# Performance work log

Hardware: AMD Instinct MI355X
Metric: run time of the kernel (lower is better)

Reference implementation:

```python
import jax, jax.numpy as jnp
import numpy as np

B, C, H, W = 16, 64, 128, 128
C8 = C // 8


def setup_inputs() -> dict:
    key = jax.random.key(0)
    ks = jax.random.split(key, 8)
    s = 0.05
    return {
        "x": jax.random.normal(ks[0], (B, C, H, W), dtype=jnp.float32),
        "Wq": jax.random.normal(ks[1], (C8, C), dtype=jnp.float32) * s,
        "bq": jax.random.normal(ks[2], (C8,), dtype=jnp.float32) * s,
        "Wk": jax.random.normal(ks[3], (C8, C), dtype=jnp.float32) * s,
        "bk": jax.random.normal(ks[4], (C8,), dtype=jnp.float32) * s,
        "Wv": jax.random.normal(ks[5], (C, C), dtype=jnp.float32) * s,
        "bv": jax.random.normal(ks[6], (C,), dtype=jnp.float32) * s,
        "gamma": jnp.zeros((1,), dtype=jnp.float32),
    }


def _criss_cross(x, Wq, bq, Wk, bk, Wv, bv, gamma):
    # 1x1 convs == channel-mixing matmuls
    q = jnp.einsum("bchw,oc->bohw", x, Wq) + bq[None, :, None, None]  # [B,C8,H,W]
    k = jnp.einsum("bchw,oc->bohw", x, Wk) + bk[None, :, None, None]  # [B,C8,H,W]
    v = jnp.einsum("bchw,oc->bohw", x, Wv) + bv[None, :, None, None]  # [B,C,H,W]

    h = x.shape[2]
    # column (H-axis) attention scores; diagonal masked to -inf
    energy_H = jnp.einsum("bchw,bciw->bhwi", q, k)  # [B,H,W,H]
    diag = jnp.eye(h, dtype=bool)[None, :, None, :]  # mask where query row == key row
    energy_H = jnp.where(diag, -jnp.inf, energy_H)
    # row (W-axis) attention scores
    energy_W = jnp.einsum("bchw,bchj->bhwj", q, k)  # [B,H,W,W]

    # joint softmax over concatenated H+W axis
    att = jax.nn.softmax(jnp.concatenate([energy_H, energy_W], axis=3), axis=3)
    att_H = att[:, :, :, :h]    # [B,H,W,H]
    att_W = att[:, :, :, h:]    # [B,H,W,W]

    out_H = jnp.einsum("bhwi,bciw->bchw", att_H, v)
    out_W = jnp.einsum("bhwj,bchj->bchw", att_W, v)
    return gamma[0] * (out_H + out_W) + x


def reference(x, Wq, bq, Wk, bk, Wv, bv, gamma):
    return _criss_cross(x, Wq, bq, Wk, bk, Wv, bv, gamma)
```

## Files before the change

kernel.cpp:

```cpp
#include <hip/hip_runtime.h>

#define HW 128
#define CC 64
#define C8V 8
#define NB 16

typedef _Float16 h1;
typedef _Float16 h2 __attribute__((ext_vector_type(2)));
typedef _Float16 half8 __attribute__((ext_vector_type(8)));
typedef float float16v __attribute__((ext_vector_type(16)));
typedef uint uv4 __attribute__((ext_vector_type(4)));

__device__ __forceinline__ uint packh2(float a, float b) {
#if __has_builtin(__builtin_amdgcn_cvt_pkrtz)
  return __builtin_bit_cast(uint, __builtin_amdgcn_cvt_pkrtz(a, b));
#else
  h2 v; v[0] = (h1)a; v[1] = (h1)b; return __builtin_bit_cast(uint, v);
#endif
}
__device__ __forceinline__ ushort f2h(float a) { h1 v = (h1)a; return __builtin_bit_cast(ushort, v); }
__device__ __forceinline__ float  h2f(ushort a) { return (float)__builtin_bit_cast(h1, a); }

__device__ __forceinline__ float16v mfma16(uv4 a, uv4 b, float16v c) {
  return __builtin_amdgcn_mfma_f32_32x32x16_f16(
      __builtin_bit_cast(half8, a), __builtin_bit_cast(half8, b), c, 0, 0, 0);
}

__global__ __launch_bounds__(256) void k_proj(
    const float* __restrict__ x,
    const float* __restrict__ Wq, const float* __restrict__ bq,
    const float* __restrict__ Wk, const float* __restrict__ bk,
    const float* __restrict__ Wv, const float* __restrict__ bv,
    ushort* __restrict__ q, ushort* __restrict__ k, ushort* __restrict__ v)
{
  alignas(16) __shared__ ushort smem[16128];
  __shared__ float bias_l[96];
  ushort* x_l = smem;
  ushort* W_l = smem + 128 * 72;

  int t = threadIdx.x;
  int lane = t & 63, wv = t >> 6;
  int b = blockIdx.x >> 7, r = blockIdx.x & 127;

  #pragma unroll
  for (int i = 0; i < 20; ++i) {
    int idx = t + 256 * i; int o_ = idx >> 6, c = idx & 63;
    float wval = (o_ < 8) ? Wq[o_ * 64 + c] : (o_ < 16) ? Wk[(o_ - 8) * 64 + c] : Wv[(o_ - 16) * 64 + c];
    W_l[o_ * 72 + c] = f2h(wval);
  }
  if (t < 96) bias_l[t] = (t < 8) ? bq[t] : (t < 16) ? bk[t - 8] : (t < 80) ? bv[t - 16] : 0.f;

  const float* xrow = x + (size_t)(b * CC) * (HW * HW) + (size_t)r * HW;
  #pragma unroll
  for (int i = 0; i < 8; ++i) {
    int idx = t + 256 * i; int c = idx >> 5, w4 = idx & 31;
    float4 xv = *(const float4*)(xrow + (size_t)c * (HW * HW) + w4 * 4);
    x_l[(w4 * 4 + 0) * 72 + c] = f2h(xv.x);
    x_l[(w4 * 4 + 1) * 72 + c] = f2h(xv.y);
    x_l[(w4 * 4 + 2) * 72 + c] = f2h(xv.z);
    x_l[(w4 * 4 + 3) * 72 + c] = f2h(xv.w);
  }
  __syncthreads();

  int w = 32 * wv + (lane & 31);
  float16v acc0 = {}, acc1 = {}, acc2 = {};
  #pragma unroll
  for (int ks = 0; ks < 4; ++ks) {
    int c0 = 8 * (lane >> 5) + 16 * ks;
    uv4 Bx = *(const uv4*)&x_l[w * 72 + c0];
    uv4 a0 = *(const uv4*)&W_l[((lane & 31) + 0) * 72 + c0];
    uv4 a1 = *(const uv4*)&W_l[((lane & 31) + 32) * 72 + c0];
    uv4 a2 = *(const uv4*)&W_l[((lane & 31) + 64) * 72 + c0];
    acc0 = mfma16(a0, Bx, acc0);
    acc1 = mfma16(a1, Bx, acc1);
    acc2 = mfma16(a2, Bx, acc2);
  }
  __syncthreads();

  ushort* o_l = smem;
  int hi = lane >> 5;
  #pragma unroll
  for (int reg = 0; reg < 16; ++reg) {
    int orow = (reg & 3) + 8 * (reg >> 2) + 4 * hi;
    o_l[(orow +  0) * 128 + w] = f2h(acc0[reg] + bias_l[orow]);
    o_l[(orow + 32) * 128 + w] = f2h(acc1[reg] + bias_l[orow + 32]);
    if (orow + 64 < 80)
      o_l[(orow + 64) * 128 + w] = f2h(acc2[reg] + bias_l[orow + 64]);
  }
  __syncthreads();

  ushort* qb = q + (size_t)(b * C8V) * (HW * HW) + (size_t)r * HW;
  ushort* kb = k + (size_t)(b * C8V) * (HW * HW) + (size_t)r * HW;
  ushort* vb = v + (size_t)(b * CC)  * (HW * HW) + (size_t)r * HW;
  #pragma unroll
  for (int i = 0; i < 5; ++i) {
    int idx = t + 256 * i; int o_ = idx >> 4, w8 = idx & 15;
    uv4 val = *(const uv4*)&o_l[o_ * 128 + w8 * 8];
    ushort* dst = (o_ < 8) ? qb + (size_t)o_ * (HW * HW)
                : (o_ < 16) ? kb + (size_t)(o_ - 8) * (HW * HW)
                            : vb + (size_t)(o_ - 16) * (HW * HW);
    *(uv4*)(dst + w8 * 8) = val;
  }
}

__global__ __launch_bounds__(256) void k_transpose_all(
    const ushort* __restrict__ q, ushort* __restrict__ qT,
    const ushort* __restrict__ k, ushort* __restrict__ kT,
    const ushort* __restrict__ v, ushort* __restrict__ vT)
{
  __shared__ ushort tl[128 * 130];
  int t = threadIdx.x;
  int p = blockIdx.x;
  const ushort* in; ushort* out;
  if (p < 128)      { size_t base = (size_t)p * (HW * HW);         in = q + base; out = qT + base; }
  else if (p < 256) { size_t base = (size_t)(p - 128) * (HW * HW); in = k + base; out = kT + base; }
  else              { size_t base = (size_t)(p - 256) * (HW * HW); in = v + base; out = vT + base; }
  const uint* ip = (const uint*)in;
  uint* op = (uint*)out;
  int c2 = t & 63;
  int r0 = t >> 6;
  for (int it = 0; it < 32; ++it) {
    int r = it * 4 + r0;
    uint val = ip[r * 64 + c2];
    *(uint*)&tl[r * 130 + c2 * 2] = val;
  }
  __syncthreads();
  for (int it = 0; it < 32; ++it) {
    int wcol = it * 4 + r0;
    int hh = c2 * 2;
    uint lo = tl[hh * 130 + wcol];
    uint hi = tl[(hh + 1) * 130 + wcol];
    op[wcol * 64 + c2] = lo | (hi << 16);
  }
}

__global__ __launch_bounds__(256) void k_attn_both(
    const ushort* __restrict__ q,  const ushort* __restrict__ kkn, const ushort* __restrict__ vn,
    const ushort* __restrict__ qT, const ushort* __restrict__ kkT, const ushort* __restrict__ vT,
    ushort* __restrict__ oW_, float* __restrict__ mW_, float* __restrict__ sW_,
    ushort* __restrict__ oH_, float* __restrict__ mH_, float* __restrict__ sH_)
{
  alignas(16) __shared__ ushort Q_l[128][16];
  alignas(16) __shared__ ushort K_l[128][16];
  alignas(16) __shared__ uint   V_l[64 * 64];

  int t = threadIdx.x;
  int lane = t & 63, wv = t >> 6;
  int hi = lane >> 5;
  int bid = blockIdx.x & 2047;
  bool maskf = blockIdx.x >= 2048;
  const ushort* qp = maskf ? qT : q;
  const ushort* kp = maskf ? kkT : kkn;
  const ushort* vp = maskf ? vT : vn;
  ushort* op = maskf ? oH_ : oW_;
  float* mo = maskf ? mH_ : mW_;
  float* so = maskf ? sH_ : sW_;

  int b = bid >> 7, r = bid & 127;
  size_t plane32 = (size_t)(HW * HW) / 2;

  if (t < 128) {
    *(uv4*)&Q_l[t][8] = (uv4){0, 0, 0, 0};
    *(uv4*)&K_l[t][8] = (uv4){0, 0, 0, 0};
  }
  const uint* qrow = (const uint*)qp + (size_t)(b * C8V) * plane32 + (size_t)r * 64;
  const uint* krow = (const uint*)kp + (size_t)(b * C8V) * plane32 + (size_t)r * 64;
  #pragma unroll
  for (int i = 0; i < 2; ++i) {
    int idx = t + 256 * i; int c = idx >> 6, w2 = idx & 63;
    uint qv = qrow[(size_t)c * plane32 + w2];
    Q_l[2 * w2][c] = (ushort)(qv & 0xffff); Q_l[2 * w2 + 1][c] = (ushort)(qv >> 16);
    uint kv = krow[(size_t)c * plane32 + w2];
    K_l[2 * w2][c] = (ushort)(kv & 0xffff); K_l[2 * w2 + 1][c] = (ushort)(kv >> 16);
  }
  const uint* vrow = (const uint*)vp + (size_t)(b * CC) * plane32 + (size_t)r * 64;
  #pragma unroll
  for (int i = 0; i < 16; ++i) {
    int idx = t + 256 * i; int c = idx >> 6, j2 = idx & 63;
    uint val = vrow[(size_t)c * plane32 + j2];
    uint byteoff = c * 256 + ((4 * j2) ^ ((c & 15) << 4));
    V_l[byteoff >> 2] = val;
  }
  __syncthreads();

  uv4 Bq = *(const uv4*)&Q_l[(lane & 31) + 32 * wv][hi * 8];
  float16v e[4];
  #pragma unroll
  for (int mt = 0; mt < 4; ++mt) {
    uv4 ka = *(const uv4*)&K_l[(lane & 31) + 32 * mt][hi * 8];
    float16v z = {};
    e[mt] = mfma16(ka, Bq, z);
  }

  int qg = 32 * wv + (lane & 31);
  float m = -INFINITY;
  #pragma unroll
  for (int mt = 0; mt < 4; ++mt) {
    #pragma unroll
    for (int reg = 0; reg < 16; ++reg) {
      float ev = e[mt][reg];
      if (maskf) {
        int key = 32 * mt + ((reg & 3) + 8 * (reg >> 2) + 4 * hi);
        ev = (key == qg) ? -INFINITY : ev;
        e[mt][reg] = ev;
      }
      m = fmaxf(m, ev);
    }
  }
  m = fmaxf(m, __shfl_xor(m, 32));
  float s = 0.f;
  #pragma unroll
  for (int mt = 0; mt < 4; ++mt) {
    #pragma unroll
    for (int reg = 0; reg < 16; ++reg) {
      float p = __expf(e[mt][reg] - m);
      e[mt][reg] = p;
      s += p;
    }
  }
  s += __shfl_xor(s, 32);
  if (lane < 32) {
    mo[(size_t)bid * HW + qg] = m;
    so[(size_t)bid * HW + qg] = s;
  }

  float16v acc0 = {}, acc1 = {};
  #pragma unroll
  for (int s8 = 0; s8 < 8; ++s8) {
    int mt = s8 >> 1, hf = s8 & 1;
    float p0 = e[mt][8 * hf + 0], p1 = e[mt][8 * hf + 1];
    float p2 = e[mt][8 * hf + 2], p3 = e[mt][8 * hf + 3];
    float p4 = e[mt][8 * hf + 4], p5 = e[mt][8 * hf + 5];
    float p6 = e[mt][8 * hf + 6], p7 = e[mt][8 * hf + 7];
    uint X = packh2(p0, p1), Y = packh2(p2, p3), Z = packh2(p4, p5), Wp = packh2(p6, p7);
    uint Xs = __shfl_xor(X, 32), Ys = __shfl_xor(Y, 32);
    uint Zs = __shfl_xor(Z, 32), Ws = __shfl_xor(Wp, 32);
    uv4 Bp;
    Bp[0] = (hi == 0) ? X  : Zs;
    Bp[1] = (hi == 0) ? Y  : Ws;
    Bp[2] = (hi == 0) ? Xs : Z;
    Bp[3] = (hi == 0) ? Ys : Wp;
    #pragma unroll
    for (int ct = 0; ct < 2; ++ct) {
      int c = (lane & 31) + 32 * ct;
      uint byteoff = c * 256 + ((16 * (hi + 2 * s8)) ^ ((c & 15) << 4));
      uv4 va = *(const uv4*)((const char*)V_l + byteoff);
      if (ct == 0) acc0 = mfma16(va, Bp, acc0);
      else         acc1 = mfma16(va, Bp, acc1);
    }
  }

  __syncthreads();
  ushort* o_l = (ushort*)V_l;
  int w = 32 * wv + (lane & 31);
  #pragma unroll
  for (int reg = 0; reg < 16; ++reg) {
    int c = (reg & 3) + 8 * (reg >> 2) + 4 * hi;
    o_l[(c +  0) * 128 + w] = f2h(acc0[reg]);
    o_l[(c + 32) * 128 + w] = f2h(acc1[reg]);
  }
  __syncthreads();
  ushort* ob = op + (size_t)(b * CC) * (HW * HW) + (size_t)r * HW;
  #pragma unroll
  for (int i = 0; i < 4; ++i) {
    int idx = t + 256 * i; int c = idx >> 4, w8 = idx & 15;
    *(uv4*)(ob + (size_t)c * (HW * HW) + w8 * 8) = *(const uv4*)&o_l[c * 128 + w8 * 8];
  }
}

__global__ __launch_bounds__(256) void k_alpha(
    const float* __restrict__ mH, const float* __restrict__ sH,
    const float* __restrict__ mW, const float* __restrict__ sW,
    ushort* __restrict__ aHT, ushort* __restrict__ aWn)
{
  __shared__ float mw_l[128 * 17], sw_l[128 * 17];
  __shared__ ushort aw_l[128 * 18];
  int t = threadIdx.x;
  int b = blockIdx.x >> 3, ws = blockIdx.x & 7;
  int w0 = ws * 16;
  const int PL = HW * HW;

  #pragma unroll
  for (int i = 0; i < 8; ++i) {
    int p = t + 256 * i;
    int w = p & 15, h = p >> 4;
    mw_l[h * 17 + w] = mW[(size_t)b * PL + h * HW + w0 + w];
    sw_l[h * 17 + w] = sW[(size_t)b * PL + h * HW + w0 + w];
  }
  __syncthreads();
  #pragma unroll
  for (int i = 0; i < 8; ++i) {
    int p = t + 256 * i;
    int h = p & 127, w = p >> 7;
    size_t tidx = (size_t)b * PL + (size_t)(w0 + w) * HW + h;
    float mh = mH[tidx], sh = sH[tidx];
    float mw = mw_l[h * 17 + w], sw = sw_l[h * 17 + w];
    float mm = fmaxf(mh, mw);
    float eh = __expf(mh - mm), ew = __expf(mw - mm);
    float inv = 1.f / (sh * eh + sw * ew);
    aHT[tidx] = f2h(eh * inv);
    aw_l[h * 18 + w] = f2h(ew * inv);
  }
  __syncthreads();
  #pragma unroll
  for (int i = 0; i < 8; ++i) {
    int p = t + 256 * i;
    int w = p & 15, h = p >> 4;
    aWn[(size_t)b * PL + (size_t)h * HW + w0 + w] = aw_l[h * 18 + w];
  }
}

__global__ __launch_bounds__(256) void k_merge(
    const ushort* __restrict__ oHT, const ushort* __restrict__ oW,
    const ushort* __restrict__ aHT, const ushort* __restrict__ aWn,
    const float* __restrict__ x, const float* __restrict__ gamma,
    float* __restrict__ out)
{
  alignas(16) __shared__ ushort otile[4 * 32 * 132];
  int t = threadIdx.x;
  int bid = blockIdx.x;
  int wsel = bid & 3, cg = (bid >> 2) & 15, b = bid >> 6;
  int w0 = wsel * 32;
  float g = gamma[0];
  const int PL = HW * HW;

  #pragma unroll
  for (int i = 0; i < 8; ++i) {
    int p = t + 256 * i;
    int ch = p >> 9, rest = p & 511;
    int w = rest >> 4, hg = rest & 15;
    size_t cbase = (size_t)(b * CC + cg * 4 + ch) * PL;
    uv4 ov = *(const uv4*)(oHT + cbase + (size_t)(w0 + w) * HW + hg * 8);
    uv4 av = *(const uv4*)(aHT + (size_t)b * PL + (size_t)(w0 + w) * HW + hg * 8);
    uv4 res;
    #pragma unroll
    for (int jj = 0; jj < 4; ++jj) {
      h2 o2 = __builtin_bit_cast(h2, ov[jj]);
      h2 a2 = __builtin_bit_cast(h2, av[jj]);
      res[jj] = __builtin_bit_cast(uint, o2 * a2);
    }
    *(uv4*)&otile[(ch * 32 + w) * 132 + hg * 8] = res;
  }
  __syncthreads();

  #pragma unroll
  for (int ch = 0; ch < 4; ++ch) {
    size_t cbase = (size_t)(b * CC + cg * 4 + ch) * PL;
    const ushort* otc = &otile[ch * 32 * 132];
    #pragma unroll
    for (int i = 0; i < 2; ++i) {
      int p = t + 256 * i;
      int w4 = p & 7, hh2 = p >> 3;
      float th0[4], th1[4];
      #pragma unroll
      for (int j = 0; j < 4; ++j) {
        uint pk = *(const uint*)&otc[(4 * w4 + j) * 132 + 2 * hh2];
        th0[j] = h2f((ushort)(pk & 0xffff));
        th1[j] = h2f((ushort)(pk >> 16));
      }
      #pragma unroll
      for (int rr = 0; rr < 2; ++rr) {
        int hh = 2 * hh2 + rr;
        const float* th = rr ? th1 : th0;
        size_t base = cbase + (size_t)hh * HW + w0 + 4 * w4;
        size_t abase = (size_t)b * PL + (size_t)hh * HW + w0 + 4 * w4;
        uint2 aw2 = *(const uint2*)(aWn + abase);
        uint2 ow2 = *(const uint2*)(oW + base);
        float4 xv = *(const float4*)(x + base);
        float4 res;
        res.x = g * (th[0] + h2f((ushort)(ow2.x & 0xffff)) * h2f((ushort)(aw2.x & 0xffff))) + xv.x;
        res.y = g * (th[1] + h2f((ushort)(ow2.x >> 16))    * h2f((ushort)(aw2.x >> 16)))    + xv.y;
        res.z = g * (th[2] + h2f((ushort)(ow2.y & 0xffff)) * h2f((ushort)(aw2.y & 0xffff))) + xv.z;
        res.w = g * (th[3] + h2f((ushort)(ow2.y >> 16))    * h2f((ushort)(aw2.y >> 16)))    + xv.w;
        *(float4*)(out + base) = res;
      }
    }
  }
}

extern "C" void kernel_launch(void* const* d_in, const int* in_sizes, int n_in,
                              void* d_out, int out_size, void* d_ws, size_t ws_size,
                              hipStream_t stream)
{
  const float* x     = (const float*)d_in[0];
  const float* Wq    = (const float*)d_in[1];
  const float* bq    = (const float*)d_in[2];
  const float* Wk    = (const float*)d_in[3];
  const float* bk    = (const float*)d_in[4];
  const float* Wv    = (const float*)d_in[5];
  const float* bv    = (const float*)d_in[6];
  const float* gamma = (const float*)d_in[7];
  float* out = (float*)d_out;

  char* w = (char*)d_ws;
  size_t np = (size_t)NB * HW * HW;
  ushort* q   = (ushort*)w;  w += np * C8V * 2;
  ushort* k   = (ushort*)w;  w += np * C8V * 2;
  ushort* qT  = (ushort*)w;  w += np * C8V * 2;
  ushort* kT  = (ushort*)w;  w += np * C8V * 2;
  ushort* v   = (ushort*)w;  w += np * CC * 2;
  ushort* vT  = (ushort*)w;  w += np * CC * 2;
  ushort* oW  = (ushort*)w;  w += np * CC * 2;
  ushort* oHT = (ushort*)w;  w += np * CC * 2;
  float* mW = (float*)w;  w += np * 4;
  float* sW = (float*)w;  w += np * 4;
  float* mH = (float*)w;  w += np * 4;
  float* sH = (float*)w;  w += np * 4;
  ushort* aHT = (ushort*)w; w += np * 2;
  ushort* aWn = (ushort*)w; w += np * 2;
  if ((size_t)(w - (char*)d_ws) > ws_size) return;

  k_proj<<<NB * HW, 256, 0, stream>>>(x, Wq, bq, Wk, bk, Wv, bv, q, k, v);
  k_transpose_all<<<256 + NB * CC, 256, 0, stream>>>(q, qT, k, kT, v, vT);
  k_attn_both<<<2 * NB * HW, 256, 0, stream>>>(q, k, v, qT, kT, vT,
                                               oW, mW, sW, oHT, mH, sH);
  k_alpha<<<NB * 8, 256, 0, stream>>>(mH, sH, mW, sW, aHT, aWn);
  k_merge<<<NB * 16 * 4, 256, 0, stream>>>(oHT, oW, aHT, aWn, x, gamma, out);
}
```

Measured before the change: 123.9 us.

## Store q/k pixel-major with zero padding to drop their transposes

The projection kernel now writes q and k in a per-pixel layout of 16 halfs (8 channels plus 8 zeros), so the attention kernel can load MFMA operands straight from global memory for both row and column passes. This removes the q/k transpose blocks and the q/k shared-memory staging in the attention kernel. The column pass now reads with a strided, less coalesced pattern, and q/k storage doubles in size because of the zero padding.

```diff
diff --git a/kernel.cpp b/kernel.cpp
--- a/kernel.cpp
+++ b/kernel.cpp
@@ -77,46 +77,50 @@
   }
   __syncthreads();
 
-  ushort* o_l = smem;
+  ushort* o_l  = smem;
+  ushort* qk_l = smem + 8192;
   int hi = lane >> 5;
+
+  {
+    int zw = t >> 1, sel = t & 1;
+    *(uv4*)&qk_l[zw * 40 + 8 + 16 * sel] = (uv4){0, 0, 0, 0};
+  }
+
   #pragma unroll
   for (int reg = 0; reg < 16; ++reg) {
     int orow = (reg & 3) + 8 * (reg >> 2) + 4 * hi;
-    o_l[(orow +  0) * 128 + w] = f2h(acc0[reg] + bias_l[orow]);
-    o_l[(orow + 32) * 128 + w] = f2h(acc1[reg] + bias_l[orow + 32]);
-    if (orow + 64 < 80)
-      o_l[(orow + 64) * 128 + w] = f2h(acc2[reg] + bias_l[orow + 64]);
-  }
-  __syncthreads();
-
-  ushort* qb = q + (size_t)(b * C8V) * (HW * HW) + (size_t)r * HW;
-  ushort* kb = k + (size_t)(b * C8V) * (HW * HW) + (size_t)r * HW;
-  ushort* vb = v + (size_t)(b * CC)  * (HW * HW) + (size_t)r * HW;
-  #pragma unroll
-  for (int i = 0; i < 5; ++i) {
+    float v0 = acc0[reg] + bias_l[orow];
+    if (orow < 8)       qk_l[w * 40 + orow] = f2h(v0);
+    else if (orow < 16) qk_l[w * 40 + 8 + orow] = f2h(v0);
+    else                o_l[(orow - 16) * 128 + w] = f2h(v0);
+    o_l[(orow + 16) * 128 + w] = f2h(acc1[reg] + bias_l[orow + 32]);
+    if (orow < 16)
+      o_l[(orow + 48) * 128 + w] = f2h(acc2[reg] + bias_l[orow + 64]);
+  }
+  __syncthreads();
+
+  size_t pixbase = (size_t)(b * HW + r) * HW * 16;
+  {
+    int pw = t >> 1, part = t & 1;
+    *(uv4*)(q + pixbase + t * 8) = *(const uv4*)&qk_l[pw * 40 + part * 8];
+    *(uv4*)(k + pixbase + t * 8) = *(const uv4*)&qk_l[pw * 40 + 16 + part * 8];
+  }
+  ushort* vb = v + (size_t)(b * CC) * (HW * HW) + (size_t)r * HW;
+  #pragma unroll
+  for (int i = 0; i < 4; ++i) {
     int idx = t + 256 * i; int o_ = idx >> 4, w8 = idx & 15;
-    uv4 val = *(const uv4*)&o_l[o_ * 128 + w8 * 8];
-    ushort* dst = (o_ < 8) ? qb + (size_t)o_ * (HW * HW)
-                : (o_ < 16) ? kb + (size_t)(o_ - 8) * (HW * HW)
-                            : vb + (size_t)(o_ - 16) * (HW * HW);
-    *(uv4*)(dst + w8 * 8) = val;
-  }
-}
-
-__global__ __launch_bounds__(256) void k_transpose_all(
-    const ushort* __restrict__ q, ushort* __restrict__ qT,
-    const ushort* __restrict__ k, ushort* __restrict__ kT,
-    const ushort* __restrict__ v, ushort* __restrict__ vT)
+    *(uv4*)(vb + (size_t)o_ * (HW * HW) + w8 * 8) = *(const uv4*)&o_l[o_ * 128 + w8 * 8];
+  }
+}
+
+__global__ __launch_bounds__(256) void k_transpose_v(const ushort* __restrict__ v,
+                                                     ushort* __restrict__ vT)
 {
   __shared__ ushort tl[128 * 130];
   int t = threadIdx.x;
-  int p = blockIdx.x;
-  const ushort* in; ushort* out;
-  if (p < 128)      { size_t base = (size_t)p * (HW * HW);         in = q + base; out = qT + base; }
-  else if (p < 256) { size_t base = (size_t)(p - 128) * (HW * HW); in = k + base; out = kT + base; }
-  else              { size_t base = (size_t)(p - 256) * (HW * HW); in = v + base; out = vT + base; }
-  const uint* ip = (const uint*)in;
-  uint* op = (uint*)out;
+  size_t base = (size_t)blockIdx.x * (HW * HW);
+  const uint* ip = (const uint*)(v + base);
+  uint* op = (uint*)(vT + base);
   int c2 = t & 63;
   int r0 = t >> 6;
   for (int it = 0; it < 32; ++it) {
@@ -135,22 +139,18 @@
 }
 
 __global__ __launch_bounds__(256) void k_attn_both(
-    const ushort* __restrict__ q,  const ushort* __restrict__ kkn, const ushort* __restrict__ vn,
-    const ushort* __restrict__ qT, const ushort* __restrict__ kkT, const ushort* __restrict__ vT,
+    const ushort* __restrict__ qpix, const ushort* __restrict__ kpix,
+    const ushort* __restrict__ vn,   const ushort* __restrict__ vT,
     ushort* __restrict__ oW_, float* __restrict__ mW_, float* __restrict__ sW_,
     ushort* __restrict__ oH_, float* __restrict__ mH_, float* __restrict__ sH_)
 {
-  alignas(16) __shared__ ushort Q_l[128][16];
-  alignas(16) __shared__ ushort K_l[128][16];
-  alignas(16) __shared__ uint   V_l[64 * 64];
+  alignas(16) __shared__ uint V_l[64 * 64];
 
   int t = threadIdx.x;
   int lane = t & 63, wv = t >> 6;
   int hi = lane >> 5;
   int bid = blockIdx.x & 2047;
   bool maskf = blockIdx.x >= 2048;
-  const ushort* qp = maskf ? qT : q;
-  const ushort* kp = maskf ? kkT : kkn;
   const ushort* vp = maskf ? vT : vn;
   ushort* op = maskf ? oH_ : oW_;
   float* mo = maskf ? mH_ : mW_;
@@ -159,20 +159,17 @@
   int b = bid >> 7, r = bid & 127;
   size_t plane32 = (size_t)(HW * HW) / 2;
 
-  if (t < 128) {
-    *(uv4*)&Q_l[t][8] = (uv4){0, 0, 0, 0};
-    *(uv4*)&K_l[t][8] = (uv4){0, 0, 0, 0};
-  }
-  const uint* qrow = (const uint*)qp + (size_t)(b * C8V) * plane32 + (size_t)r * 64;
-  const uint* krow = (const uint*)kp + (size_t)(b * C8V) * plane32 + (size_t)r * 64;
-  #pragma unroll
-  for (int i = 0; i < 2; ++i) {
-    int idx = t + 256 * i; int c = idx >> 6, w2 = idx & 63;
-    uint qv = qrow[(size_t)c * plane32 + w2];
-    Q_l[2 * w2][c] = (ushort)(qv & 0xffff); Q_l[2 * w2 + 1][c] = (ushort)(qv >> 16);
-    uint kv = krow[(size_t)c * plane32 + w2];
-    K_l[2 * w2][c] = (ushort)(kv & 0xffff); K_l[2 * w2 + 1][c] = (ushort)(kv >> 16);
-  }
+  size_t pixbase; int strideJ;
+  if (!maskf) { pixbase = (size_t)(b * HW + r) * HW * 16; strideJ = 16; }
+  else        { pixbase = ((size_t)(b * HW) * HW + r) * 16; strideJ = HW * 16; }
+
+  int qg = 32 * wv + (lane & 31);
+  uv4 Bq = *(const uv4*)(qpix + pixbase + (size_t)qg * strideJ + hi * 8);
+  uv4 ka[4];
+  #pragma unroll
+  for (int mt = 0; mt < 4; ++mt)
+    ka[mt] = *(const uv4*)(kpix + pixbase + (size_t)((lane & 31) + 32 * mt) * strideJ + hi * 8);
+
   const uint* vrow = (const uint*)vp + (size_t)(b * CC) * plane32 + (size_t)r * 64;
   #pragma unroll
   for (int i = 0; i < 16; ++i) {
@@ -183,16 +180,13 @@
   }
   __syncthreads();
 
-  uv4 Bq = *(const uv4*)&Q_l[(lane & 31) + 32 * wv][hi * 8];
   float16v e[4];
   #pragma unroll
   for (int mt = 0; mt < 4; ++mt) {
-    uv4 ka = *(const uv4*)&K_l[(lane & 31) + 32 * mt][hi * 8];
     float16v z = {};
-    e[mt] = mfma16(ka, Bq, z);
-  }
-
-  int qg = 32 * wv + (lane & 31);
+    e[mt] = mfma16(ka[mt], Bq, z);
+  }
+
   float m = -INFINITY;
   #pragma unroll
   for (int mt = 0; mt < 4; ++mt) {
@@ -394,10 +388,8 @@
 
   char* w = (char*)d_ws;
   size_t np = (size_t)NB * HW * HW;
-  ushort* q   = (ushort*)w;  w += np * C8V * 2;
-  ushort* k   = (ushort*)w;  w += np * C8V * 2;
-  ushort* qT  = (ushort*)w;  w += np * C8V * 2;
-  ushort* kT  = (ushort*)w;  w += np * C8V * 2;
+  ushort* q   = (ushort*)w;  w += np * 16 * 2;
+  ushort* k   = (ushort*)w;  w += np * 16 * 2;
   ushort* v   = (ushort*)w;  w += np * CC * 2;
   ushort* vT  = (ushort*)w;  w += np * CC * 2;
   ushort* oW  = (ushort*)w;  w += np * CC * 2;
@@ -411,8 +403,8 @@
   if ((size_t)(w - (char*)d_ws) > ws_size) return;
 
   k_proj<<<NB * HW, 256, 0, stream>>>(x, Wq, bq, Wk, bk, Wv, bv, q, k, v);
-  k_transpose_all<<<256 + NB * CC, 256, 0, stream>>>(q, qT, k, kT, v, vT);
-  k_attn_both<<<2 * NB * HW, 256, 0, stream>>>(q, k, v, qT, kT, vT,
+  k_transpose_v<<<NB * CC, 256, 0, stream>>>(v, vT);
+  k_attn_both<<<2 * NB * HW, 256, 0, stream>>>(q, k, v, vT,
                                                oW, mW, sW, oHT, mH, sH);
   k_alpha<<<NB * 8, 256, 0, stream>>>(mH, sH, mW, sW, aHT, aWn);
   k_merge<<<NB * 16 * 4, 256, 0, stream>>>(oHT, oW, aHT, aWn, x, gamma, out);
```

Result: slower. 129.3 us (+4.4%).
